# Kernel optimization log

Hardware: AMD Instinct MI355X
Metric: run time of the kernel (lower is better)

Reference implementation:

```python
import jax, jax.numpy as jnp
import numpy as np

DECAY = 0.9      # LIF membrane decay per step
V_TH = 1.0       # spike threshold


def setup_inputs() -> dict:
    key = jax.random.key(0)
    k1, k2, k3, k4, k5 = jax.random.split(key, 5)
    B, D, N = 256, 1024, 2048
    density = 0.3
    external_inputs = jax.random.normal(k1, (B, D), dtype=jnp.float32)
    # nn.Linear(input_dim, num_neurons): weight [N, D], bias [N]
    W_in = jax.random.normal(k2, (N, D), dtype=jnp.float32) / np.sqrt(D)
    b_in = jnp.zeros((N,), dtype=jnp.float32)
    adj_weights = jax.random.normal(k3, (N, N), dtype=jnp.float32) * 0.01
    mask = (jax.random.uniform(k4, (N, N)) < density).astype(jnp.float32)
    mask = mask * (1.0 - jnp.eye(N, dtype=jnp.float32))  # zero diagonal
    return {
        "external_inputs": external_inputs,
        "W_in": W_in,
        "b_in": b_in,
        "adj_weights": adj_weights,
        "mask": mask,
        "time_steps": 64,
    }


def _spike(x):
    # Heaviside spike: 1 if membrane exceeds threshold
    return (x >= 0.0).astype(x.dtype)


def reference(external_inputs, W_in, b_in, adj_weights, mask, time_steps):
    B = external_inputs.shape[0]
    N = adj_weights.shape[0]
    I_ext = external_inputs @ W_in.T + b_in              # [B, N]
    W_eff = adj_weights * mask                           # [N, N]
    V0 = jnp.zeros((B, N), dtype=external_inputs.dtype)
    s0 = jnp.zeros((B, N), dtype=external_inputs.dtype)

    def step(carry, _):
        V, s = carry
        I_total = I_ext + s @ W_eff.T                    # recurrent current
        V = DECAY * V + I_total                          # LIF integration
        s_new = _spike(V - V_TH)
        V = V * (1.0 - s_new)                            # reset on spike
        return (V, s_new), s_new

    (_, _), spike_hist = jax.lax.scan(step, (V0, s0), None, length=time_steps)
    return spike_hist.mean(axis=0)                       # [B, N] firing rates
```

## Files before the change

### kernel.cpp

```cpp
#include <hip/hip_runtime.h>
#include <cstdint>
#include <cstddef>

#define N_NEU 2048
#define D_IN  1024
#define T_STEPS 64

typedef _Float16 f16x8 __attribute__((ext_vector_type(8)));
typedef _Float16 f16x4 __attribute__((ext_vector_type(4)));
typedef float    f32x4 __attribute__((ext_vector_type(4)));
typedef float    f32x16 __attribute__((ext_vector_type(16)));
typedef unsigned u32x4 __attribute__((ext_vector_type(4)));

#define MFMA32(a, b, c) __builtin_amdgcn_mfma_f32_32x32x16_f16((a), (b), (c), 0, 0, 0)


__device__ inline f16x8 expand8(unsigned b) {
  u32x4 t;
#pragma unroll
  for (int i = 0; i < 4; ++i) {
    unsigned m = (b >> (2 * i)) & 3u;
    unsigned s = (m | (m << 15)) & 0x00010001u;
    t[i] = s * 0x3C00u;
  }
  return __builtin_bit_cast(f16x8, t);
}

__global__ __launch_bounds__(256) void k_wsplit(const float* __restrict__ adj,
                                                const float* __restrict__ mask,
                                                _Float16* __restrict__ Wh,
                                                _Float16* __restrict__ Wl,
                                                unsigned long long* __restrict__ bmv) {
  const int idx = blockIdx.x * 256 + threadIdx.x;
  if (idx < 2 * 256 * 64) bmv[idx] = 0ull;
  const int total4 = (N_NEU * N_NEU) / 4;
  for (int i = idx; i < total4; i += gridDim.x * 256) {
    float4 a = ((const float4*)adj)[i];
    float4 m = ((const float4*)mask)[i];
    float w0 = a.x * m.x, w1 = a.y * m.y, w2 = a.z * m.z, w3 = a.w * m.w;
    f16x4 h, lo;
    h[0] = (_Float16)w0; lo[0] = (_Float16)((w0 - (float)h[0]) * 4096.0f);
    h[1] = (_Float16)w1; lo[1] = (_Float16)((w1 - (float)h[1]) * 4096.0f);
    h[2] = (_Float16)w2; lo[2] = (_Float16)((w2 - (float)h[2]) * 4096.0f);
    h[3] = (_Float16)w3; lo[3] = (_Float16)((w3 - (float)h[3]) * 4096.0f);
    ((f16x4*)Wh)[i] = h;
    ((f16x4*)Wl)[i] = lo;
  }
}

__global__ __launch_bounds__(256) void k_iext(const float* __restrict__ ext,
                                              const float* __restrict__ Win,
                                              const float* __restrict__ bin,
                                              float* __restrict__ Iext) {
  __shared__ float At[32][68];
  __shared__ float Bt[32][68];
  const int tid = threadIdx.x;
  const int b0 = (blockIdx.x & 3) * 64;
  const int n0 = (blockIdx.x >> 2) * 64;
  const int tx = tid & 15, ty = tid >> 4;
  float acc[4][4] = {};
  for (int kt = 0; kt < D_IN / 32; ++kt) {
    const int k0 = kt * 32;
#pragma unroll
    for (int i = 0; i < 8; ++i) {
      int e = tid + i * 256;
      int kk = e & 31, row = e >> 5;
      At[kk][row] = ext[(size_t)(b0 + row) * D_IN + k0 + kk];
      Bt[kk][row] = Win[(size_t)(n0 + row) * D_IN + k0 + kk];
    }
    __syncthreads();
    for (int kk = 0; kk < 32; ++kk) {
      f32x4 a = *(const f32x4*)&At[kk][ty * 4];
      f32x4 b = *(const f32x4*)&Bt[kk][tx * 4];
#pragma unroll
      for (int i = 0; i < 4; ++i)
#pragma unroll
        for (int j = 0; j < 4; ++j) acc[i][j] += a[i] * b[j];
    }
    __syncthreads();
  }
#pragma unroll
  for (int i = 0; i < 4; ++i)
#pragma unroll
    for (int j = 0; j < 4; ++j)
      Iext[(size_t)(b0 + ty * 4 + i) * N_NEU + n0 + tx * 4 + j] = acc[i][j] + bin[n0 + tx * 4 + j];
}

__global__ __launch_bounds__(512, 2) void k_fused13(
    const _Float16* __restrict__ Wh, const _Float16* __restrict__ Wl,
    const float* __restrict__ Iext, unsigned long long* __restrict__ bmv,
    float* __restrict__ out) {
  __shared__ float red[8 * 32 * 33];
  __shared__ unsigned bmA[32 * 64];
  __shared__ unsigned bmB[32 * 64];

  const int tid = threadIdx.x;
  const int lane = tid & 63;
  const int kw = tid >> 6;
  const int l31 = lane & 31;
  const int hl = lane >> 5;
  const int gp = blockIdx.x >> 6;
  const int ns = blockIdx.x & 63;
  const int n0 = ns * 32;
  const int gA = gp, gB = gp + 4;
  const float inv4096 = 1.0f / 4096.0f;

  float IxA[2], IxB[2];
#pragma unroll
  for (int j = 0; j < 2; ++j) {
    IxA[j] = Iext[(size_t)(gA * 32 + j * 16 + (tid >> 5)) * N_NEU + n0 + (tid & 31)];
    IxB[j] = Iext[(size_t)(gB * 32 + j * 16 + (tid >> 5)) * N_NEU + n0 + (tid & 31)];
  }

  const _Float16* whb = Wh + (size_t)(n0 + l31) * N_NEU + kw * 256 + hl * 8;
  const _Float16* wlb = Wl + (size_t)(n0 + l31) * N_NEU + kw * 256 + hl * 8;
  f16x8 whf[16], wlf[16];
#pragma unroll
  for (int kcl = 0; kcl < 16; ++kcl) {
    whf[kcl] = *(const f16x8*)(whb + kcl * 16);
    wlf[kcl] = *(const f16x8*)(wlb + kcl * 16);
  }

  float VA[2] = {0.f, 0.f}, VB[2] = {0.f, 0.f};
  unsigned cA[2] = {0u, 0u}, cB[2] = {0u, 0u};
  unsigned long long vA[4], vB[4];

  auto spec_issue = [&](int g, int buf, unsigned long long (&v)[4]) {
    const unsigned long long* src = bmv + (size_t)buf * 16384 + (size_t)g * 2048 + tid;
#pragma unroll
    for (int i = 0; i < 4; ++i)
      v[i] = __hip_atomic_load(src + (size_t)i * 512, __ATOMIC_RELAXED, __HIP_MEMORY_SCOPE_AGENT);
  };
  auto check_retry = [&](int g, int buf, unsigned want, unsigned long long (&v)[4]) {
    const unsigned long long* src = bmv + (size_t)buf * 16384 + (size_t)g * 2048 + tid;
    unsigned need = 0u;
#pragma unroll
    for (int i = 0; i < 4; ++i)
      if ((unsigned)(v[i] >> 32) != want) need |= 1u << i;
    while (need) {
      __builtin_amdgcn_s_sleep(2);
#pragma unroll
      for (int i = 0; i < 4; ++i)
        if (need & (1u << i)) {
          v[i] = __hip_atomic_load(src + (size_t)i * 512,
                                   __ATOMIC_RELAXED, __HIP_MEMORY_SCOPE_AGENT);
          if ((unsigned)(v[i] >> 32) == want) need &= ~(1u << i);
        }
    }
  };
  auto stage = [&](unsigned* bm, const unsigned long long (&v)[4]) {
#pragma unroll
    for (int i = 0; i < 4; ++i) {
      const int w = i * 512 + tid, r = w >> 6, nsw = w & 63;
      bm[r * 64 + (nsw ^ ((r & 15) << 2))] = (unsigned)v[i];
    }
  };
  auto gemm = [&](const unsigned* bm, float (&cI)[2]) {
    f32x16 acch = {0.f, 0.f, 0.f, 0.f, 0.f, 0.f, 0.f, 0.f,
                   0.f, 0.f, 0.f, 0.f, 0.f, 0.f, 0.f, 0.f};
    f32x16 accl = acch;
    const int arow = l31;
    const int swz = (arow & 15) << 2;
    const u32x4 q0 = *(const u32x4*)&bm[arow * 64 + ((kw * 8) ^ swz)];
    const u32x4 q1 = *(const u32x4*)&bm[arow * 64 + (((kw * 8) | 4) ^ swz)];
    const unsigned sh0 = hl * 8;
#pragma unroll
    for (int kcl = 0; kcl < 16; ++kcl) {
      const unsigned word = (kcl < 8) ? q0[kcl >> 1] : q1[(kcl >> 1) - 4];
      const f16x8 a = expand8((word >> (sh0 + ((kcl & 1) << 4))) & 0xFFu);
      acch = MFMA32(a, whf[kcl], acch);
      accl = MFMA32(a, wlf[kcl], accl);
    }
    f32x16 cb = acch + accl * inv4096;
    const int hl4 = hl * 4;
#pragma unroll
    for (int rg = 0; rg < 4; ++rg) {
      f32x4 part = {cb[rg * 4 + 0], cb[rg * 4 + 1], cb[rg * 4 + 2], cb[rg * 4 + 3]};
      *(f32x4*)&red[(kw * 32 + l31) * 33 + rg * 8 + hl4] = part;
    }
    __syncthreads();
#pragma unroll
    for (int j = 0; j < 2; ++j) {
      const int o = j * 512 + tid;
      const int row = o >> 5, col = o & 31;
      float s = 0.0f;
#pragma unroll
      for (int p = 0; p < 8; ++p) s += red[(p * 32 + col) * 33 + row];
      cI[j] = s;
    }
  };
  auto lif = [&](const float (&cI)[2], const float (&Ix)[2], float (&V)[2],
                 unsigned (&cnt)[2], int g, int nbuf, unsigned tag, bool dostore) {
#pragma unroll
    for (int j = 0; j < 2; ++j) {
      float I = cI[j] + Ix[j];
      float v = 0.9f * V[j] + I;
      bool sp = (v - 1.0f) >= 0.0f;
      V[j] = sp ? 0.0f : v;
      cnt[j] += sp ? 1u : 0u;
      if (dostore) {
        unsigned long long ba = __ballot(sp);
        const int rowf = g * 32 + j * 16 + kw * 2;
        const unsigned long long tg = ((unsigned long long)tag) << 32;
        if (lane == 0)
          __hip_atomic_store(bmv + (size_t)nbuf * 16384 + (size_t)rowf * 64 + ns,
                             tg | (unsigned)ba, __ATOMIC_RELAXED, __HIP_MEMORY_SCOPE_AGENT);
        else if (lane == 32)
          __hip_atomic_store(bmv + (size_t)nbuf * 16384 + (size_t)(rowf + 1) * 64 + ns,
                             tg | (unsigned)(ba >> 32), __ATOMIC_RELAXED, __HIP_MEMORY_SCOPE_AGENT);
      }
    }
  };

  {
    const float cz[2] = {0.f, 0.f};
    lif(cz, IxA, VA, cA, gA, 1, 1u, true);
    lif(cz, IxB, VB, cB, gB, 1, 1u, true);
    spec_issue(gA, 1, vA);
  }

  for (int t = 1; t < T_STEPS; ++t) {
    const int cbuf = t & 1, nbuf = (t + 1) & 1;
    const bool last = (t == T_STEPS - 1);
    float cI[2];

    check_retry(gA, cbuf, (unsigned)t, vA);
    stage(bmA, vA);
    __syncthreads();
    spec_issue(gB, cbuf, vB);
    gemm(bmA, cI);
    lif(cI, IxA, VA, cA, gA, nbuf, (unsigned)(t + 1), !last);

    check_retry(gB, cbuf, (unsigned)t, vB);
    stage(bmB, vB);
    __syncthreads();
    if (!last) spec_issue(gA, nbuf, vA);
    gemm(bmB, cI);
    lif(cI, IxB, VB, cB, gB, nbuf, (unsigned)(t + 1), !last);
  }

#pragma unroll
  for (int j = 0; j < 2; ++j) {
    const int rA = gA * 32 + j * 16 + (tid >> 5);
    const int rB = gB * 32 + j * 16 + (tid >> 5);
    out[(size_t)rA * N_NEU + n0 + (tid & 31)] = (float)cA[j] * 0.015625f;
    out[(size_t)rB * N_NEU + n0 + (tid & 31)] = (float)cB[j] * 0.015625f;
  }
}

extern "C" void kernel_launch(void* const* d_in, const int* in_sizes, int n_in,
                              void* d_out, int out_size, void* d_ws, size_t ws_size,
                              hipStream_t stream) {
  (void)in_sizes; (void)n_in; (void)out_size; (void)ws_size;
  const float* ext  = (const float*)d_in[0];
  const float* Win  = (const float*)d_in[1];
  const float* bin  = (const float*)d_in[2];
  const float* adj  = (const float*)d_in[3];
  const float* mask = (const float*)d_in[4];
  unsigned char* ws = (unsigned char*)d_ws;

  _Float16* Wh   = (_Float16*)(ws);
  _Float16* Wl   = (_Float16*)(ws + (size_t)(8u << 20));
  float*    Iext = (float*)   (ws + (size_t)(16u << 20));
  unsigned long long* bmv = (unsigned long long*)(ws + (size_t)(18u << 20));
  float* out = (float*)d_out;

  hipLaunchKernelGGL(k_wsplit, dim3(2048), dim3(256), 0, stream, adj, mask, Wh, Wl, bmv);
  hipLaunchKernelGGL(k_iext,   dim3(128),  dim3(256), 0, stream, ext, Win, bin, Iext);
  hipLaunchKernelGGL(k_fused13, dim3(256), dim3(512), 0, stream,
                     Wh, Wl, Iext, bmv, out);
}
```

Before: 393.7 us.

## Transpose spike bitmask layout so lanes read MFMA operands directly from global

Reorganizes the global spike bitmap so each lane's atomic loads yield exactly the bits it needs for its MFMA A-operand. This removes the LDS staging step and one __syncthreads per half-step. The weight fragment K mapping changes to match, and the reduction buffer is double-buffered so consecutive gemms do not race. It also raises wave priority around the MFMA loop and shortens the spin sleep, which may add polling traffic.

```diff
diff --git a/kernel.cpp b/kernel.cpp
--- a/kernel.cpp
+++ b/kernel.cpp
@@ -32,7 +32,7 @@
                                                 _Float16* __restrict__ Wl,
                                                 unsigned long long* __restrict__ bmv) {
   const int idx = blockIdx.x * 256 + threadIdx.x;
-  if (idx < 2 * 256 * 64) bmv[idx] = 0ull;
+  if (idx < 2 * 64 * 256) bmv[idx] = 0ull;
   const int total4 = (N_NEU * N_NEU) / 4;
   for (int i = idx; i < total4; i += gridDim.x * 256) {
     float4 a = ((const float4*)adj)[i];
@@ -86,13 +86,11 @@
       Iext[(size_t)(b0 + ty * 4 + i) * N_NEU + n0 + tx * 4 + j] = acc[i][j] + bin[n0 + tx * 4 + j];
 }
 
-__global__ __launch_bounds__(512, 2) void k_fused13(
+__global__ __launch_bounds__(512, 2) void k_fused14(
     const _Float16* __restrict__ Wh, const _Float16* __restrict__ Wl,
     const float* __restrict__ Iext, unsigned long long* __restrict__ bmv,
     float* __restrict__ out) {
-  __shared__ float red[8 * 32 * 33];
-  __shared__ unsigned bmA[32 * 64];
-  __shared__ unsigned bmB[32 * 64];
+  __shared__ float red[2][8 * 32 * 33];
 
   const int tid = threadIdx.x;
   const int lane = tid & 63;
@@ -112,13 +110,13 @@
     IxB[j] = Iext[(size_t)(gB * 32 + j * 16 + (tid >> 5)) * N_NEU + n0 + (tid & 31)];
   }
 
-  const _Float16* whb = Wh + (size_t)(n0 + l31) * N_NEU + kw * 256 + hl * 8;
-  const _Float16* wlb = Wl + (size_t)(n0 + l31) * N_NEU + kw * 256 + hl * 8;
+  const _Float16* whb = Wh + (size_t)(n0 + l31) * N_NEU + kw * 256 + hl * 128;
+  const _Float16* wlb = Wl + (size_t)(n0 + l31) * N_NEU + kw * 256 + hl * 128;
   f16x8 whf[16], wlf[16];
 #pragma unroll
   for (int kcl = 0; kcl < 16; ++kcl) {
-    whf[kcl] = *(const f16x8*)(whb + kcl * 16);
-    wlf[kcl] = *(const f16x8*)(wlb + kcl * 16);
+    whf[kcl] = *(const f16x8*)(whb + kcl * 8);
+    wlf[kcl] = *(const f16x8*)(wlb + kcl * 8);
   }
 
   float VA[2] = {0.f, 0.f}, VB[2] = {0.f, 0.f};
@@ -126,57 +124,51 @@
   unsigned long long vA[4], vB[4];
 
   auto spec_issue = [&](int g, int buf, unsigned long long (&v)[4]) {
-    const unsigned long long* src = bmv + (size_t)buf * 16384 + (size_t)g * 2048 + tid;
+    const unsigned long long* src =
+        bmv + (size_t)buf * 16384 + (size_t)(kw * 8 + hl * 4) * 256 + gp * 64 + g * 32 + l31;
 #pragma unroll
     for (int i = 0; i < 4; ++i)
-      v[i] = __hip_atomic_load(src + (size_t)i * 512, __ATOMIC_RELAXED, __HIP_MEMORY_SCOPE_AGENT);
+      v[i] = __hip_atomic_load(src + (size_t)i * 256, __ATOMIC_RELAXED, __HIP_MEMORY_SCOPE_AGENT);
   };
   auto check_retry = [&](int g, int buf, unsigned want, unsigned long long (&v)[4]) {
-    const unsigned long long* src = bmv + (size_t)buf * 16384 + (size_t)g * 2048 + tid;
+    const unsigned long long* src =
+        bmv + (size_t)buf * 16384 + (size_t)(kw * 8 + hl * 4) * 256 + gp * 64 + g * 32 + l31;
     unsigned need = 0u;
 #pragma unroll
     for (int i = 0; i < 4; ++i)
       if ((unsigned)(v[i] >> 32) != want) need |= 1u << i;
     while (need) {
-      __builtin_amdgcn_s_sleep(2);
+      __builtin_amdgcn_s_sleep(1);
 #pragma unroll
       for (int i = 0; i < 4; ++i)
         if (need & (1u << i)) {
-          v[i] = __hip_atomic_load(src + (size_t)i * 512,
+          v[i] = __hip_atomic_load(src + (size_t)i * 256,
                                    __ATOMIC_RELAXED, __HIP_MEMORY_SCOPE_AGENT);
           if ((unsigned)(v[i] >> 32) == want) need &= ~(1u << i);
         }
     }
   };
-  auto stage = [&](unsigned* bm, const unsigned long long (&v)[4]) {
-#pragma unroll
-    for (int i = 0; i < 4; ++i) {
-      const int w = i * 512 + tid, r = w >> 6, nsw = w & 63;
-      bm[r * 64 + (nsw ^ ((r & 15) << 2))] = (unsigned)v[i];
-    }
-  };
-  auto gemm = [&](const unsigned* bm, float (&cI)[2]) {
+  auto gemm = [&](const unsigned long long (&v)[4], float* redb, float (&cI)[2]) {
+    unsigned q[4];
+#pragma unroll
+    for (int i = 0; i < 4; ++i) q[i] = (unsigned)v[i];
     f32x16 acch = {0.f, 0.f, 0.f, 0.f, 0.f, 0.f, 0.f, 0.f,
                    0.f, 0.f, 0.f, 0.f, 0.f, 0.f, 0.f, 0.f};
     f32x16 accl = acch;
-    const int arow = l31;
-    const int swz = (arow & 15) << 2;
-    const u32x4 q0 = *(const u32x4*)&bm[arow * 64 + ((kw * 8) ^ swz)];
-    const u32x4 q1 = *(const u32x4*)&bm[arow * 64 + (((kw * 8) | 4) ^ swz)];
-    const unsigned sh0 = hl * 8;
+    __builtin_amdgcn_s_setprio(1);
 #pragma unroll
     for (int kcl = 0; kcl < 16; ++kcl) {
-      const unsigned word = (kcl < 8) ? q0[kcl >> 1] : q1[(kcl >> 1) - 4];
-      const f16x8 a = expand8((word >> (sh0 + ((kcl & 1) << 4))) & 0xFFu);
+      const f16x8 a = expand8((q[kcl >> 2] >> ((kcl & 3) * 8)) & 0xFFu);
       acch = MFMA32(a, whf[kcl], acch);
       accl = MFMA32(a, wlf[kcl], accl);
     }
+    __builtin_amdgcn_s_setprio(0);
     f32x16 cb = acch + accl * inv4096;
     const int hl4 = hl * 4;
 #pragma unroll
     for (int rg = 0; rg < 4; ++rg) {
       f32x4 part = {cb[rg * 4 + 0], cb[rg * 4 + 1], cb[rg * 4 + 2], cb[rg * 4 + 3]};
-      *(f32x4*)&red[(kw * 32 + l31) * 33 + rg * 8 + hl4] = part;
+      *(f32x4*)&redb[(kw * 32 + l31) * 33 + rg * 8 + hl4] = part;
     }
     __syncthreads();
 #pragma unroll
@@ -185,7 +177,7 @@
       const int row = o >> 5, col = o & 31;
       float s = 0.0f;
 #pragma unroll
-      for (int p = 0; p < 8; ++p) s += red[(p * 32 + col) * 33 + row];
+      for (int p = 0; p < 8; ++p) s += redb[(p * 32 + col) * 33 + row];
       cI[j] = s;
     }
   };
@@ -200,23 +192,24 @@
       cnt[j] += sp ? 1u : 0u;
       if (dostore) {
         unsigned long long ba = __ballot(sp);
-        const int rowf = g * 32 + j * 16 + kw * 2;
+        const int rowf = gp * 64 + g * 32 + j * 16 + kw * 2;
         const unsigned long long tg = ((unsigned long long)tag) << 32;
+        unsigned long long* dst = bmv + (size_t)nbuf * 16384 + (size_t)ns * 256;
         if (lane == 0)
-          __hip_atomic_store(bmv + (size_t)nbuf * 16384 + (size_t)rowf * 64 + ns,
-                             tg | (unsigned)ba, __ATOMIC_RELAXED, __HIP_MEMORY_SCOPE_AGENT);
+          __hip_atomic_store(dst + rowf, tg | (unsigned)ba,
+                             __ATOMIC_RELAXED, __HIP_MEMORY_SCOPE_AGENT);
         else if (lane == 32)
-          __hip_atomic_store(bmv + (size_t)nbuf * 16384 + (size_t)(rowf + 1) * 64 + ns,
-                             tg | (unsigned)(ba >> 32), __ATOMIC_RELAXED, __HIP_MEMORY_SCOPE_AGENT);
+          __hip_atomic_store(dst + rowf + 1, tg | (unsigned)(ba >> 32),
+                             __ATOMIC_RELAXED, __HIP_MEMORY_SCOPE_AGENT);
       }
     }
   };
 
   {
     const float cz[2] = {0.f, 0.f};
-    lif(cz, IxA, VA, cA, gA, 1, 1u, true);
-    lif(cz, IxB, VB, cB, gB, 1, 1u, true);
-    spec_issue(gA, 1, vA);
+    lif(cz, IxA, VA, cA, 0, 1, 1u, true);
+    lif(cz, IxB, VB, cB, 1, 1, 1u, true);
+    spec_issue(0, 1, vA);
   }
 
   for (int t = 1; t < T_STEPS; ++t) {
@@ -224,19 +217,15 @@
     const bool last = (t == T_STEPS - 1);
     float cI[2];
 
-    check_retry(gA, cbuf, (unsigned)t, vA);
-    stage(bmA, vA);
-    __syncthreads();
-    spec_issue(gB, cbuf, vB);
-    gemm(bmA, cI);
-    lif(cI, IxA, VA, cA, gA, nbuf, (unsigned)(t + 1), !last);
-
-    check_retry(gB, cbuf, (unsigned)t, vB);
-    stage(bmB, vB);
-    __syncthreads();
-    if (!last) spec_issue(gA, nbuf, vA);
-    gemm(bmB, cI);
-    lif(cI, IxB, VB, cB, gB, nbuf, (unsigned)(t + 1), !last);
+    check_retry(0, cbuf, (unsigned)t, vA);
+    spec_issue(1, cbuf, vB);
+    gemm(vA, red[0], cI);
+    lif(cI, IxA, VA, cA, 0, nbuf, (unsigned)(t + 1), !last);
+
+    check_retry(1, cbuf, (unsigned)t, vB);
+    if (!last) spec_issue(0, nbuf, vA);
+    gemm(vB, red[1], cI);
+    lif(cI, IxB, VB, cB, 1, nbuf, (unsigned)(t + 1), !last);
   }
 
 #pragma unroll
@@ -267,6 +256,6 @@
 
   hipLaunchKernelGGL(k_wsplit, dim3(2048), dim3(256), 0, stream, adj, mask, Wh, Wl, bmv);
   hipLaunchKernelGGL(k_iext,   dim3(128),  dim3(256), 0, stream, ext, Win, bin, Iext);
-  hipLaunchKernelGGL(k_fused13, dim3(256), dim3(512), 0, stream,
+  hipLaunchKernelGGL(k_fused14, dim3(256), dim3(512), 0, stream,
                      Wh, Wl, Iext, bmv, out);
 }
```

After: 544.0 us. +38.2%, slower.

## Move high-half recurrent weights from registers into LDS and share staging buffer

Applied to the files above, without the earlier changes.

The high-precision fp16 half of each block's 32-column weight slice now lives in a 128KB LDS array instead of 16 VGPR vectors per thread, cutting register pressure. The spike bitmap and reduction scratch now share one pool, which costs extra barriers per half-step. The reduction layout changes from a padded stride to an XOR swizzle, and the MFMA loop is raised in wave priority. In exchange, every MFMA step reads its weights from LDS, and with 160KB of LDS per block occupancy may be limited to one block per CU, which risks hurting the persistent 256-block grid that relies on co-residency for its spin-waits.

```diff
diff --git a/kernel.cpp b/kernel.cpp
--- a/kernel.cpp
+++ b/kernel.cpp
@@ -86,13 +86,12 @@
       Iext[(size_t)(b0 + ty * 4 + i) * N_NEU + n0 + tx * 4 + j] = acc[i][j] + bin[n0 + tx * 4 + j];
 }
 
-__global__ __launch_bounds__(512, 2) void k_fused13(
+__global__ __launch_bounds__(512, 2) void k_fused17(
     const _Float16* __restrict__ Wh, const _Float16* __restrict__ Wl,
     const float* __restrict__ Iext, unsigned long long* __restrict__ bmv,
     float* __restrict__ out) {
-  __shared__ float red[8 * 32 * 33];
-  __shared__ unsigned bmA[32 * 64];
-  __shared__ unsigned bmB[32 * 64];
+  __shared__ _Float16 WhL[65536];
+  __shared__ float pool[8192];
 
   const int tid = threadIdx.x;
   const int lane = tid & 63;
@@ -104,6 +103,14 @@
   const int n0 = ns * 32;
   const int gA = gp, gB = gp + 4;
   const float inv4096 = 1.0f / 4096.0f;
+  unsigned* bm = (unsigned*)pool;
+
+#pragma unroll
+  for (int i = 0; i < 16; ++i) {
+    const int c = i * 512 + tid;
+    const int col = c >> 8, k8 = c & 255;
+    ((f16x8*)WhL)[k8 * 32 + col] = *(const f16x8*)(Wh + (size_t)(n0 + col) * N_NEU + k8 * 8);
+  }
 
   float IxA[2], IxB[2];
 #pragma unroll
@@ -112,14 +119,10 @@
     IxB[j] = Iext[(size_t)(gB * 32 + j * 16 + (tid >> 5)) * N_NEU + n0 + (tid & 31)];
   }
 
-  const _Float16* whb = Wh + (size_t)(n0 + l31) * N_NEU + kw * 256 + hl * 8;
   const _Float16* wlb = Wl + (size_t)(n0 + l31) * N_NEU + kw * 256 + hl * 8;
-  f16x8 whf[16], wlf[16];
-#pragma unroll
-  for (int kcl = 0; kcl < 16; ++kcl) {
-    whf[kcl] = *(const f16x8*)(whb + kcl * 16);
-    wlf[kcl] = *(const f16x8*)(wlb + kcl * 16);
-  }
+  f16x8 wlf[16];
+#pragma unroll
+  for (int kcl = 0; kcl < 16; ++kcl) wlf[kcl] = *(const f16x8*)(wlb + kcl * 16);
 
   float VA[2] = {0.f, 0.f}, VB[2] = {0.f, 0.f};
   unsigned cA[2] = {0u, 0u}, cB[2] = {0u, 0u};
@@ -148,44 +151,49 @@
         }
     }
   };
-  auto stage = [&](unsigned* bm, const unsigned long long (&v)[4]) {
+  auto stage = [&](const unsigned long long (&v)[4]) {
 #pragma unroll
     for (int i = 0; i < 4; ++i) {
       const int w = i * 512 + tid, r = w >> 6, nsw = w & 63;
       bm[r * 64 + (nsw ^ ((r & 15) << 2))] = (unsigned)v[i];
     }
   };
-  auto gemm = [&](const unsigned* bm, float (&cI)[2]) {
-    f32x16 acch = {0.f, 0.f, 0.f, 0.f, 0.f, 0.f, 0.f, 0.f,
-                   0.f, 0.f, 0.f, 0.f, 0.f, 0.f, 0.f, 0.f};
-    f32x16 accl = acch;
-    const int arow = l31;
-    const int swz = (arow & 15) << 2;
-    const u32x4 q0 = *(const u32x4*)&bm[arow * 64 + ((kw * 8) ^ swz)];
-    const u32x4 q1 = *(const u32x4*)&bm[arow * 64 + (((kw * 8) | 4) ^ swz)];
+  auto gemm = [&](float (&cI)[2]) {
+    const f32x16 z16 = {0.f, 0.f, 0.f, 0.f, 0.f, 0.f, 0.f, 0.f,
+                        0.f, 0.f, 0.f, 0.f, 0.f, 0.f, 0.f, 0.f};
+    f32x16 acch = z16, accl = z16;
+    const int swz = (l31 & 15) << 2;
+    const u32x4 q0 = *(const u32x4*)&bm[l31 * 64 + ((kw * 8) ^ swz)];
+    const u32x4 q1 = *(const u32x4*)&bm[l31 * 64 + (((kw * 8) | 4) ^ swz)];
     const unsigned sh0 = hl * 8;
+    __syncthreads();
+    __builtin_amdgcn_s_setprio(1);
 #pragma unroll
     for (int kcl = 0; kcl < 16; ++kcl) {
       const unsigned word = (kcl < 8) ? q0[kcl >> 1] : q1[(kcl >> 1) - 4];
       const f16x8 a = expand8((word >> (sh0 + ((kcl & 1) << 4))) & 0xFFu);
-      acch = MFMA32(a, whf[kcl], acch);
+      const f16x8 wh = *(const f16x8*)&WhL[((kw * 32 + kcl * 2 + hl) * 32 + l31) * 8];
+      acch = MFMA32(a, wh, acch);
       accl = MFMA32(a, wlf[kcl], accl);
     }
+    __builtin_amdgcn_s_setprio(0);
     f32x16 cb = acch + accl * inv4096;
     const int hl4 = hl * 4;
+    const int xr = (l31 & 7) << 2;
 #pragma unroll
     for (int rg = 0; rg < 4; ++rg) {
       f32x4 part = {cb[rg * 4 + 0], cb[rg * 4 + 1], cb[rg * 4 + 2], cb[rg * 4 + 3]};
-      *(f32x4*)&red[(kw * 32 + l31) * 33 + rg * 8 + hl4] = part;
+      *(f32x4*)&pool[(kw * 32 + l31) * 32 + ((rg * 8 + hl4) ^ xr)] = part;
     }
     __syncthreads();
 #pragma unroll
     for (int j = 0; j < 2; ++j) {
       const int o = j * 512 + tid;
       const int row = o >> 5, col = o & 31;
+      const int rs = row ^ ((col & 7) << 2);
       float s = 0.0f;
 #pragma unroll
-      for (int p = 0; p < 8; ++p) s += red[(p * 32 + col) * 33 + row];
+      for (int p = 0; p < 8; ++p) s += pool[(p * 32 + col) * 32 + rs];
       cI[j] = s;
     }
   };
@@ -225,17 +233,19 @@
     float cI[2];
 
     check_retry(gA, cbuf, (unsigned)t, vA);
-    stage(bmA, vA);
+    __syncthreads();
+    stage(vA);
     __syncthreads();
     spec_issue(gB, cbuf, vB);
-    gemm(bmA, cI);
+    gemm(cI);
     lif(cI, IxA, VA, cA, gA, nbuf, (unsigned)(t + 1), !last);
 
     check_retry(gB, cbuf, (unsigned)t, vB);
-    stage(bmB, vB);
+    __syncthreads();
+    stage(vB);
     __syncthreads();
     if (!last) spec_issue(gA, nbuf, vA);
-    gemm(bmB, cI);
+    gemm(cI);
     lif(cI, IxB, VB, cB, gB, nbuf, (unsigned)(t + 1), !last);
   }
 
@@ -267,6 +277,6 @@
 
   hipLaunchKernelGGL(k_wsplit, dim3(2048), dim3(256), 0, stream, adj, mask, Wh, Wl, bmv);
   hipLaunchKernelGGL(k_iext,   dim3(128),  dim3(256), 0, stream, ext, Win, bin, Iext);
-  hipLaunchKernelGGL(k_fused13, dim3(256), dim3(512), 0, stream,
+  hipLaunchKernelGGL(k_fused17, dim3(256), dim3(512), 0, stream,
                      Wh, Wl, Iext, bmv, out);
 }
```

Measured after the change: 436.4 us. 1.11x slower.
